# Optimization experiments

Hardware: AMD Instinct MI355X
Metric: run time of the kernel (lower is better)

## Reference

```python
import jax, jax.numpy as jnp
import numpy as np

N_FILLERS = 10000
N_ROLES = 256
FILLER_DIM = 256
ROLE_DIM = 256
HIDDEN = 1024
B, S = 64, 128


def setup_inputs() -> dict:
    key = jax.random.key(0)
    k1, k2, k3, k4, k5, k6 = jax.random.split(key, 6)
    roles = jax.random.randint(k1, (B, S), 0, N_ROLES, dtype=jnp.int64 if jax.config.jax_enable_x64 else jnp.int32)
    hidden = jax.random.normal(k2, (1, B, HIDDEN), dtype=jnp.float32)
    filler_emb = jax.random.normal(k3, (N_FILLERS, FILLER_DIM), dtype=jnp.float32)
    role_emb = jax.random.normal(k4, (N_ROLES, ROLE_DIM), dtype=jnp.float32)
    role_emb = role_emb.at[0].set(0.0)  # padding_idx=0
    W = jax.random.normal(k5, (FILLER_DIM * ROLE_DIM, HIDDEN), dtype=jnp.float32) / np.sqrt(HIDDEN)
    b = jax.random.normal(k6, (FILLER_DIM * ROLE_DIM,), dtype=jnp.float32) * 0.01
    return {"roles": roles, "hidden": hidden, "filler_emb": filler_emb, "role_emb": role_emb, "W": W, "b": b}


def reference(roles, hidden, filler_emb, role_emb, W, b):
    fd = filler_emb.shape[1]
    rd = role_emb.shape[1]
    # input_layer: (1, B, hidden) -> (1, B, fd*rd)
    h = hidden @ W.T + b
    # transpose(0,1).transpose(1,2).view(-1, fd, rd): (B, fd, rd)
    h = jnp.transpose(h, (1, 2, 0)).reshape(-1, fd, rd)
    # role embedding with padding_idx=0 (row 0 is zero)
    role_table = role_emb.at[0].set(0.0)
    roles_e = role_table[roles]  # (B, S, rd)
    # bmm(roles_emb, hidden^T): (B, S, rd) x (B, rd, fd) -> (B, S, fd)
    fg = jnp.einsum('bsr,bfr->bsf', roles_e, h)
    # L2 distance to filler codebook via squared-norm trick: (B, S, n_fillers)
    d2 = (jnp.sum(fg * fg, axis=-1, keepdims=True)
          - 2.0 * jnp.einsum('bsf,nf->bsn', fg, filler_emb)
          + jnp.sum(filler_emb * filler_emb, axis=-1))
    dists = jnp.sqrt(jnp.maximum(d2, 0.0))
    log_probs = jax.nn.log_softmax(-dists, axis=-1)  # (B, S, n_fillers)
    preds = jnp.argmax(log_probs, axis=-1)  # top-1 indices, (B, S)
    return log_probs, preds
```

## Files before the change

kernel.cpp:

```cpp
#include <hip/hip_runtime.h>
#include <hip/hip_bf16.h>
#include <float.h>
#include <math.h>

#define ROWS 8192
#define NF   10000
#define NPAD 10240

typedef short s8v __attribute__((ext_vector_type(8)));
typedef float f4v __attribute__((ext_vector_type(4)));

#define GLD16(g, l) __builtin_amdgcn_global_load_lds((const __attribute__((address_space(1))) void*)(g), (__attribute__((address_space(3))) void*)(l), 16, 0, 0)

__device__ inline unsigned short f2bf(float x) {
  __hip_bfloat16 h = __float2bfloat16(x);
  return __builtin_bit_cast(unsigned short, h);
}
__device__ inline float bf2f(unsigned short u) {
  __hip_bfloat16 h = __builtin_bit_cast(__hip_bfloat16, u);
  return __bfloat162float(h);
}

__global__ __launch_bounds__(256) void k_cvt_filler(const float* __restrict__ filler,
                                                    unsigned short* __restrict__ fl2,
                                                    float* __restrict__ fln) {
  int row = blockIdx.x * 4 + (threadIdx.x >> 6);
  int lane = threadIdx.x & 63;
  if (row >= NPAD) return;
  if (row < NF) {
    float4 v = reinterpret_cast<const float4*>(filler + (size_t)row * 256)[lane];
    float s = v.x * v.x + v.y * v.y + v.z * v.z + v.w * v.w;
    #pragma unroll
    for (int off = 32; off >= 1; off >>= 1) s += __shfl_xor(s, off, 64);
    if (lane == 0) fln[row] = s;
    float xs[4] = {v.x, v.y, v.z, v.w};
    unsigned short h[4], lo[4];
    #pragma unroll
    for (int j = 0; j < 4; ++j) { h[j] = f2bf(xs[j]); lo[j] = f2bf(xs[j] - bf2f(h[j])); }
    uint2 hh = make_uint2(h[0] | ((unsigned)h[1] << 16), h[2] | ((unsigned)h[3] << 16));
    uint2 ll = make_uint2(lo[0] | ((unsigned)lo[1] << 16), lo[2] | ((unsigned)lo[3] << 16));
    *reinterpret_cast<uint2*>(fl2 + (size_t)row * 512 + lane * 4) = hh;
    *reinterpret_cast<uint2*>(fl2 + (size_t)row * 512 + 256 + lane * 4) = ll;
  } else {
    *reinterpret_cast<uint2*>(fl2 + (size_t)row * 512 + lane * 4) = make_uint2(0, 0);
    *reinterpret_cast<uint2*>(fl2 + (size_t)row * 512 + 256 + lane * 4) = make_uint2(0, 0);
    if (lane == 0) fln[row] = 1e30f;
  }
}

__global__ __launch_bounds__(256) void k_gemm1(const float* __restrict__ hidden,
                                               const float* __restrict__ W,
                                               const float* __restrict__ bias,
                                               float* __restrict__ ht) {
  __shared__ float As[64][68];
  __shared__ float Bs[64][136];
  __shared__ float biasS[128];
  const int tid = threadIdx.x;
  const int nbase = blockIdx.x * 128;
  const int r = nbase >> 8;
  const int f0 = nbase & 255;
  const int tm = tid >> 4, tn = tid & 15;
  const int m0 = tm * 4, n0 = tn * 8;

  if (tid < 128) biasS[tid] = bias[(size_t)(f0 + tid) * 256 + r];

  float acc[4][8];
  #pragma unroll
  for (int i = 0; i < 4; ++i)
    #pragma unroll
    for (int j = 0; j < 8; ++j) acc[i][j] = 0.f;

  for (int kt = 0; kt < 16; ++kt) {
    __syncthreads();
    #pragma unroll
    for (int i = 0; i < 4; ++i) {
      int q = tid + i * 256;
      int b = q >> 4, kq = q & 15;
      float4 v = *reinterpret_cast<const float4*>(hidden + (size_t)b * 1024 + kt * 64 + kq * 4);
      As[kq * 4 + 0][b] = v.x;
      As[kq * 4 + 1][b] = v.y;
      As[kq * 4 + 2][b] = v.z;
      As[kq * 4 + 3][b] = v.w;
    }
    #pragma unroll
    for (int i = 0; i < 8; ++i) {
      int q = tid + i * 256;
      int nl = q >> 4, kq = q & 15;
      size_t wrow = (size_t)(f0 + nl) * 256 + r;
      float4 v = *reinterpret_cast<const float4*>(W + wrow * 1024 + kt * 64 + kq * 4);
      Bs[kq * 4 + 0][nl] = v.x;
      Bs[kq * 4 + 1][nl] = v.y;
      Bs[kq * 4 + 2][nl] = v.z;
      Bs[kq * 4 + 3][nl] = v.w;
    }
    __syncthreads();
    #pragma unroll
    for (int kk = 0; kk < 64; ++kk) {
      float4 a  = *reinterpret_cast<const float4*>(&As[kk][m0]);
      float4 b0 = *reinterpret_cast<const float4*>(&Bs[kk][n0]);
      float4 b1 = *reinterpret_cast<const float4*>(&Bs[kk][n0 + 4]);
      float av[4] = {a.x, a.y, a.z, a.w};
      float bv[8] = {b0.x, b0.y, b0.z, b0.w, b1.x, b1.y, b1.z, b1.w};
      #pragma unroll
      for (int i = 0; i < 4; ++i)
        #pragma unroll
        for (int j = 0; j < 8; ++j) acc[i][j] += av[i] * bv[j];
    }
  }
  #pragma unroll
  for (int i = 0; i < 4; ++i) {
    int b = m0 + i;
    float4 o0 = make_float4(acc[i][0] + biasS[n0 + 0], acc[i][1] + biasS[n0 + 1],
                            acc[i][2] + biasS[n0 + 2], acc[i][3] + biasS[n0 + 3]);
    float4 o1 = make_float4(acc[i][4] + biasS[n0 + 4], acc[i][5] + biasS[n0 + 5],
                            acc[i][6] + biasS[n0 + 6], acc[i][7] + biasS[n0 + 7]);
    float* p = ht + (size_t)b * 65536 + nbase + n0;
    *reinterpret_cast<float4*>(p)     = o0;
    *reinterpret_cast<float4*>(p + 4) = o1;
  }
}

__global__ __launch_bounds__(256) void k_fg2(const int* __restrict__ roles,
                                             const float* __restrict__ role_emb,
                                             const float* __restrict__ ht,
                                             unsigned short* __restrict__ fg2,
                                             float* __restrict__ fgn) {
  __shared__ float As[64][40];
  __shared__ float Bs[64][264];
  __shared__ int sidx[32];
  const int tid = threadIdx.x;
  const int b = blockIdx.x >> 2;
  const int sbase = (blockIdx.x & 3) * 32;
  const int tm = tid >> 5, tn = tid & 31;
  const int m0 = tm * 4, n0 = tn * 8;
  if (tid < 32) sidx[tid] = roles[b * 128 + sbase + tid];

  float acc[4][8];
  #pragma unroll
  for (int i = 0; i < 4; ++i)
    #pragma unroll
    for (int j = 0; j < 8; ++j) acc[i][j] = 0.f;

  for (int kt = 0; kt < 4; ++kt) {
    __syncthreads();
    #pragma unroll
    for (int i = 0; i < 2; ++i) {
      int q = tid + i * 256;
      int s = q >> 4, rq = q & 15;
      float4 v = *reinterpret_cast<const float4*>(role_emb + (size_t)sidx[s] * 256 + kt * 64 + rq * 4);
      As[rq * 4 + 0][s] = v.x;
      As[rq * 4 + 1][s] = v.y;
      As[rq * 4 + 2][s] = v.z;
      As[rq * 4 + 3][s] = v.w;
    }
    #pragma unroll
    for (int i = 0; i < 16; ++i) {
      int q = tid + i * 256;
      int rr = q >> 6, fq = q & 63;
      float4 v = *reinterpret_cast<const float4*>(ht + (size_t)b * 65536 + (size_t)(kt * 64 + rr) * 256 + fq * 4);
      *reinterpret_cast<float4*>(&Bs[rr][fq * 4]) = v;
    }
    __syncthreads();
    #pragma unroll
    for (int kk = 0; kk < 64; ++kk) {
      float4 a  = *reinterpret_cast<const float4*>(&As[kk][m0]);
      float4 b0 = *reinterpret_cast<const float4*>(&Bs[kk][n0]);
      float4 b1 = *reinterpret_cast<const float4*>(&Bs[kk][n0 + 4]);
      float av[4] = {a.x, a.y, a.z, a.w};
      float bv[8] = {b0.x, b0.y, b0.z, b0.w, b1.x, b1.y, b1.z, b1.w};
      #pragma unroll
      for (int i = 0; i < 4; ++i)
        #pragma unroll
        for (int j = 0; j < 8; ++j) acc[i][j] += av[i] * bv[j];
    }
  }
  #pragma unroll
  for (int i = 0; i < 4; ++i) {
    const int grow = b * 128 + sbase + m0 + i;
    float nrm = 0.f;
    unsigned int hp[4], lp[4];
    #pragma unroll
    for (int j = 0; j < 8; j += 2) {
      float x0 = acc[i][j], x1 = acc[i][j + 1];
      nrm += x0 * x0 + x1 * x1;
      unsigned short h0 = f2bf(x0), h1 = f2bf(x1);
      unsigned short l0 = f2bf(x0 - bf2f(h0)), l1 = f2bf(x1 - bf2f(h1));
      hp[j >> 1] = h0 | ((unsigned)h1 << 16);
      lp[j >> 1] = l0 | ((unsigned)l1 << 16);
    }
    *reinterpret_cast<uint4*>(fg2 + (size_t)grow * 512 + n0)       = make_uint4(hp[0], hp[1], hp[2], hp[3]);
    *reinterpret_cast<uint4*>(fg2 + (size_t)grow * 512 + 256 + n0) = make_uint4(lp[0], lp[1], lp[2], lp[3]);
    #pragma unroll
    for (int msk = 1; msk <= 16; msk <<= 1) nrm += __shfl_xor(nrm, msk, 64);
    if (tn == 0) fgn[grow] = nrm;
  }
}

__global__ __launch_bounds__(512, 4) void k_dist(const unsigned short* __restrict__ fg2,
                                                 const unsigned short* __restrict__ fl2,
                                                 const float* __restrict__ fgn,
                                                 const float* __restrict__ fln,
                                                 float* __restrict__ out) {
  __shared__ __align__(16) char lds[2][32768];
  __shared__ float rn2s[128];
  const int tid = threadIdx.x;
  const int w = tid >> 6, l = tid & 63;
  const int g = l >> 4, lr = l & 15;
  const int mt  = (blockIdx.x & 7) * 8 + ((blockIdx.x >> 3) & 7);
  const int grp = blockIdx.x >> 6;
  const int rbase = mt << 7;
  const int wm = (w >> 2) << 6;
  const int wn = (w & 3) << 5;

  if (tid < 128) rn2s[tid] = fgn[rbase + tid];

  int rowC[2], swC[2];
  #pragma unroll
  for (int t = 0; t < 2; ++t) {
    int p = tid + t * 512;
    int row = p >> 3, c = p & 7;
    rowC[t] = row;
    swC[t] = (c ^ (row & 7)) << 3;
  }
  int offA[4], offB[2];
  #pragma unroll
  for (int i = 0; i < 4; ++i) { int r = wm + i * 16 + lr; offA[i] = r * 128 + ((g ^ (r & 7)) << 4); }
  #pragma unroll
  for (int j = 0; j < 2; ++j) { int r = wn + j * 16 + lr; offB[j] = 16384 + r * 128 + ((g ^ (r & 7)) << 4); }

  auto kAof = [](int kt) { return ((kt & 3) << 6) + ((kt >= 4 && kt < 8) ? 256 : 0); };
  auto kBof = [](int kt) { return ((kt & 3) << 6) + ((kt >= 8) ? 256 : 0); };

  auto stage = [&](int buf, int kt, int nb) {
    const int kA = kAof(kt), kB = kBof(kt);
    char* bA = &lds[buf][0]     + w * 1024;
    char* bB = &lds[buf][16384] + w * 1024;
    #pragma unroll
    for (int t = 0; t < 2; ++t) {
      GLD16(fg2 + ((size_t)(rbase + rowC[t]) * 512 + kA + swC[t]), bA + t * 8192);
      GLD16(fl2 + ((size_t)(nb    + rowC[t]) * 512 + kB + swC[t]), bB + t * 8192);
    }
  };

  stage(0, 0, grp << 7);
  __syncthreads();

  for (int s = 0; s < 10; ++s) {
    const int nt = grp + s * 8;
    const int nbase = nt << 7;
    float cnr[2];
    #pragma unroll
    for (int j = 0; j < 2; ++j) cnr[j] = fln[nbase + wn + j * 16 + lr];

    f4v acc[4][2];
    #pragma unroll
    for (int i = 0; i < 4; ++i)
      #pragma unroll
      for (int j = 0; j < 2; ++j) acc[i][j] = (f4v)0.f;

    for (int kt = 0; kt < 12; ++kt) {
      if (kt < 11)      stage((kt + 1) & 1, kt + 1, nbase);
      else if (s < 9)   stage(0, 0, (nt + 8) << 7);
      const char* A = lds[kt & 1];
      #pragma unroll
      for (int s2 = 0; s2 < 2; ++s2) {
        s8v va[4], vb[2];
        #pragma unroll
        for (int i = 0; i < 4; ++i) va[i] = *reinterpret_cast<const s8v*>(A + (offA[i] ^ (s2 << 6)));
        #pragma unroll
        for (int j = 0; j < 2; ++j) vb[j] = *reinterpret_cast<const s8v*>(A + (offB[j] ^ (s2 << 6)));
        #pragma unroll
        for (int i = 0; i < 4; ++i)
          #pragma unroll
          for (int j = 0; j < 2; ++j)
            acc[i][j] = __builtin_amdgcn_mfma_f32_16x16x32_bf16(va[i], vb[j], acc[i][j], 0, 0, 0);
      }
      __syncthreads();
    }

    float* scr = reinterpret_cast<float*>(&lds[1][0]);
    const int rem = NF - nbase;
    const int c4lim = (rem >= 128) ? 32 : (rem > 0 ? (rem >> 2) : 0);
    const int lbase = (wm >> 6) << 4;

    #pragma unroll
    for (int i = 0; i < 4; ++i) {
      #pragma unroll
      for (int j = 0; j < 2; ++j) {
        const int cloc = wn + (j << 4) + lr;
        #pragma unroll
        for (int r = 0; r < 4; ++r) {
          const int lrow = lbase + (g << 2) + r;
          const float r2 = rn2s[wm + (i << 4) + (g << 2) + r];
          float d = sqrtf(fmaxf(r2 - 2.0f * acc[i][j][r] + cnr[j], 0.f));
          scr[lrow * 132 + cloc] = d;
        }
      }
      __syncthreads();
      #pragma unroll
      for (int t2 = 0; t2 < 2; ++t2) {
        const int id2 = tid + (t2 << 9);
        const int rr2 = id2 >> 5, c4 = id2 & 31;
        f4v v = *reinterpret_cast<const f4v*>(scr + rr2 * 132 + (c4 << 2));
        if (c4 < c4lim) {
          const int grow = rbase + ((rr2 < 16) ? ((i << 4) + rr2) : (64 + (i << 4) + rr2 - 16));
          __builtin_nontemporal_store(v, reinterpret_cast<f4v*>(out + (size_t)grow * NF + nbase + (c4 << 2)));
        }
      }
      __syncthreads();
    }
  }
}

__global__ __launch_bounds__(256) void k_final(float* __restrict__ out) {
  const int row = blockIdx.x;
  __shared__ __align__(16) float rowd[10000];
  __shared__ float red[16];
  const int t = threadIdx.x;
  const int w = t >> 6, l = t & 63;
  float* po = out + (size_t)row * NF;

  float bd = FLT_MAX; int bi = 0;
  for (int c = t; c < 2500; c += 256) {
    f4v v = __builtin_nontemporal_load(reinterpret_cast<const f4v*>(po) + c);
    *reinterpret_cast<f4v*>(&rowd[c * 4]) = v;
    const int base = c * 4;
    if (v[0] < bd) { bd = v[0]; bi = base; }
    if (v[1] < bd) { bd = v[1]; bi = base + 1; }
    if (v[2] < bd) { bd = v[2]; bi = base + 2; }
    if (v[3] < bd) { bd = v[3]; bi = base + 3; }
  }
  #pragma unroll
  for (int msk = 1; msk <= 32; msk <<= 1) {
    float od = __shfl_xor(bd, msk, 64);
    int   oi = __shfl_xor(bi, msk, 64);
    if (od < bd || (od == bd && oi < bi)) { bd = od; bi = oi; }
  }
  if (l == 0) { red[w * 2] = bd; red[w * 2 + 1] = (float)bi; }
  __syncthreads();
  if (t == 0) {
    float m = red[0], mi = red[1];
    #pragma unroll
    for (int c = 1; c < 4; ++c) {
      float od = red[c * 2], oi = red[c * 2 + 1];
      if (od < m || (od == m && oi < mi)) { m = od; mi = oi; }
    }
    red[8] = m; red[9] = mi;
  }
  __syncthreads();
  const float m = red[8];

  float s = 0.f;
  for (int c = t; c < 2500; c += 256) {
    f4v v = *reinterpret_cast<const f4v*>(&rowd[c * 4]);
    s += __expf(m - v[0]) + __expf(m - v[1]) + __expf(m - v[2]) + __expf(m - v[3]);
  }
  #pragma unroll
  for (int msk = 1; msk <= 32; msk <<= 1) s += __shfl_xor(s, msk, 64);
  if (l == 0) red[10 + w] = s;
  __syncthreads();
  if (t == 0) {
    float S = red[10] + red[11] + red[12] + red[13];
    red[14] = logf(S) - m;
    out[(size_t)ROWS * NF + row] = red[9];
  }
  __syncthreads();
  const float L = red[14];

  for (int c = t; c < 2500; c += 256) {
    f4v v = *reinterpret_cast<const f4v*>(&rowd[c * 4]);
    v = -v - L;
    __builtin_nontemporal_store(v, reinterpret_cast<f4v*>(po) + c);
  }
}

extern "C" void kernel_launch(void* const* d_in, const int* in_sizes, int n_in,
                              void* d_out, int out_size, void* d_ws, size_t ws_size,
                              hipStream_t stream) {
  const int*   roles   = (const int*)d_in[0];
  const float* hidden  = (const float*)d_in[1];
  const float* filler  = (const float*)d_in[2];
  const float* roleemb = (const float*)d_in[3];
  const float* W       = (const float*)d_in[4];
  const float* bias    = (const float*)d_in[5];
  float* out = (float*)d_out;

  float* ws = (float*)d_ws;
  float*          ht    = ws;
  unsigned short* fg2   = (unsigned short*)(ws + 4194304);
  unsigned short* fl2   = (unsigned short*)(ws + 6291456);
  float*          fgn   = ws + 8912896;
  float*          fln   = fgn + 8192;

  k_cvt_filler<<<2560, 256, 0, stream>>>(filler, fl2, fln);
  k_gemm1<<<512, 256, 0, stream>>>(hidden, W, bias, ht);
  k_fg2<<<256, 256, 0, stream>>>(roles, roleemb, ht, fg2, fgn);
  k_dist<<<512, 512, 0, stream>>>(fg2, fl2, fgn, fln, out);
  k_final<<<8192, 256, 0, stream>>>(out);
}
```

Before: 525.5 us.

## Split K across wave groups with 64x64 warp tiles and LDS reduction

Warps now each own a 64x64 output tile. The two 4-wave groups each handle one half of every 64-wide K slice, so fewer LDS fragment loads are needed per MFMA. The partial accumulators are combined through LDS before the distance epilogue. The cost is more accumulator registers (64 floats per lane), an extra reduction pass with two barriers, only half the waves doing epilogue work, and the next tile's prefetch moving after the reduction, which takes away its overlap with the last K step.

```diff
diff --git a/kernel.cpp b/kernel.cpp
--- a/kernel.cpp
+++ b/kernel.cpp
@@ -209,8 +209,10 @@
   const int mt  = (blockIdx.x & 7) * 8 + ((blockIdx.x >> 3) & 7);
   const int grp = blockIdx.x >> 6;
   const int rbase = mt << 7;
-  const int wm = (w >> 2) << 6;
-  const int wn = (w & 3) << 5;
+  const int kg = w >> 2;
+  const int wq = w & 3;
+  const int wm = (wq >> 1) << 6;
+  const int wn = (wq & 1) << 6;
 
   if (tid < 128) rn2s[tid] = fgn[rbase + tid];
 
@@ -222,11 +224,11 @@
     rowC[t] = row;
     swC[t] = (c ^ (row & 7)) << 3;
   }
-  int offA[4], offB[2];
-  #pragma unroll
-  for (int i = 0; i < 4; ++i) { int r = wm + i * 16 + lr; offA[i] = r * 128 + ((g ^ (r & 7)) << 4); }
-  #pragma unroll
-  for (int j = 0; j < 2; ++j) { int r = wn + j * 16 + lr; offB[j] = 16384 + r * 128 + ((g ^ (r & 7)) << 4); }
+  int offA[4], offB[4];
+  #pragma unroll
+  for (int i = 0; i < 4; ++i) { int r = wm + i * 16 + lr; offA[i] = (r * 128 + ((g ^ (r & 7)) << 4)) ^ (kg << 6); }
+  #pragma unroll
+  for (int j = 0; j < 4; ++j) { int r = wn + j * 16 + lr; offB[j] = (16384 + r * 128 + ((g ^ (r & 7)) << 4)) ^ (kg << 6); }
 
   auto kAof = [](int kt) { return ((kt & 3) << 6) + ((kt >= 4 && kt < 8) ? 256 : 0); };
   auto kBof = [](int kt) { return ((kt & 3) << 6) + ((kt >= 8) ? 256 : 0); };
@@ -242,41 +244,58 @@
     }
   };
 
+  const int prowbase = (g << 2) ^ ((lr & 7) << 3);
+  float* quad = reinterpret_cast<float*>(&lds[0][0]) + wq * 4096;
+
   stage(0, 0, grp << 7);
   __syncthreads();
 
   for (int s = 0; s < 10; ++s) {
     const int nt = grp + s * 8;
     const int nbase = nt << 7;
-    float cnr[2];
-    #pragma unroll
-    for (int j = 0; j < 2; ++j) cnr[j] = fln[nbase + wn + j * 16 + lr];
-
-    f4v acc[4][2];
+    float cnr[4];
+    #pragma unroll
+    for (int j = 0; j < 4; ++j) cnr[j] = fln[nbase + wn + (j << 4) + lr];
+
+    f4v acc[4][4];
     #pragma unroll
     for (int i = 0; i < 4; ++i)
       #pragma unroll
-      for (int j = 0; j < 2; ++j) acc[i][j] = (f4v)0.f;
+      for (int j = 0; j < 4; ++j) acc[i][j] = (f4v)0.f;
 
     for (int kt = 0; kt < 12; ++kt) {
-      if (kt < 11)      stage((kt + 1) & 1, kt + 1, nbase);
-      else if (s < 9)   stage(0, 0, (nt + 8) << 7);
+      if (kt < 11) stage((kt + 1) & 1, kt + 1, nbase);
       const char* A = lds[kt & 1];
-      #pragma unroll
-      for (int s2 = 0; s2 < 2; ++s2) {
-        s8v va[4], vb[2];
-        #pragma unroll
-        for (int i = 0; i < 4; ++i) va[i] = *reinterpret_cast<const s8v*>(A + (offA[i] ^ (s2 << 6)));
-        #pragma unroll
-        for (int j = 0; j < 2; ++j) vb[j] = *reinterpret_cast<const s8v*>(A + (offB[j] ^ (s2 << 6)));
-        #pragma unroll
-        for (int i = 0; i < 4; ++i)
-          #pragma unroll
-          for (int j = 0; j < 2; ++j)
-            acc[i][j] = __builtin_amdgcn_mfma_f32_16x16x32_bf16(va[i], vb[j], acc[i][j], 0, 0, 0);
-      }
+      s8v va[4], vb[4];
+      #pragma unroll
+      for (int i = 0; i < 4; ++i) va[i] = *reinterpret_cast<const s8v*>(A + offA[i]);
+      #pragma unroll
+      for (int j = 0; j < 4; ++j) vb[j] = *reinterpret_cast<const s8v*>(A + offB[j]);
+      #pragma unroll
+      for (int i = 0; i < 4; ++i)
+        #pragma unroll
+        for (int j = 0; j < 4; ++j)
+          acc[i][j] = __builtin_amdgcn_mfma_f32_16x16x32_bf16(va[i], vb[j], acc[i][j], 0, 0, 0);
       __syncthreads();
     }
+
+    if (kg == 1) {
+      #pragma unroll
+      for (int i = 0; i < 4; ++i)
+        #pragma unroll
+        for (int j = 0; j < 4; ++j)
+          *reinterpret_cast<f4v*>(quad + ((j << 4) + lr) * 64 + ((i << 4) ^ prowbase)) = acc[i][j];
+    }
+    __syncthreads();
+    if (kg == 0) {
+      #pragma unroll
+      for (int i = 0; i < 4; ++i)
+        #pragma unroll
+        for (int j = 0; j < 4; ++j)
+          acc[i][j] += *reinterpret_cast<const f4v*>(quad + ((j << 4) + lr) * 64 + ((i << 4) ^ prowbase));
+    }
+    __syncthreads();
+    if (s < 9) stage(0, 0, (nt + 8) << 7);
 
     float* scr = reinterpret_cast<float*>(&lds[1][0]);
     const int rem = NF - nbase;
@@ -285,15 +304,17 @@
 
     #pragma unroll
     for (int i = 0; i < 4; ++i) {
-      #pragma unroll
-      for (int j = 0; j < 2; ++j) {
-        const int cloc = wn + (j << 4) + lr;
-        #pragma unroll
-        for (int r = 0; r < 4; ++r) {
-          const int lrow = lbase + (g << 2) + r;
-          const float r2 = rn2s[wm + (i << 4) + (g << 2) + r];
-          float d = sqrtf(fmaxf(r2 - 2.0f * acc[i][j][r] + cnr[j], 0.f));
-          scr[lrow * 132 + cloc] = d;
+      if (kg == 0) {
+        #pragma unroll
+        for (int j = 0; j < 4; ++j) {
+          const int cloc = wn + (j << 4) + lr;
+          #pragma unroll
+          for (int r = 0; r < 4; ++r) {
+            const int lrow = lbase + (g << 2) + r;
+            const float r2 = rn2s[wm + (i << 4) + (g << 2) + r];
+            float d = sqrtf(fmaxf(r2 - 2.0f * acc[i][j][r] + cnr[j], 0.f));
+            scr[lrow * 132 + cloc] = d;
+          }
         }
       }
       __syncthreads();
```

New measurement: 671.4 us. +27.8%, slower.
